# Kernel tuning notes

Hardware: AMD Instinct MI355X
Metric: run time of the kernel (lower is better)

## Reference

```python
import math
import jax, jax.numpy as jnp
import numpy as np

D_MODEL = 1024
H_HEADS = 16
D_K = D_MODEL // H_HEADS


def setup_inputs() -> dict:
    key = jax.random.key(0)
    ks = jax.random.split(key, 7)
    B, L = 4, 2048
    q = jax.random.normal(ks[0], (B, L, D_MODEL), dtype=jnp.float32)
    k = jax.random.normal(ks[1], (B, L, D_MODEL), dtype=jnp.float32)
    v = jax.random.normal(ks[2], (B, L, D_MODEL), dtype=jnp.float32)
    mask = jnp.ones((1, L, L), dtype=jnp.int32)
    # nn.Linear(d_model, d_model, bias=False) weights, shape (out, in)
    s = 1.0 / math.sqrt(D_MODEL)
    W_q = jax.random.uniform(ks[3], (D_MODEL, D_MODEL), jnp.float32, -s, s)
    W_k = jax.random.uniform(ks[4], (D_MODEL, D_MODEL), jnp.float32, -s, s)
    W_v = jax.random.uniform(ks[5], (D_MODEL, D_MODEL), jnp.float32, -s, s)
    W_o = jax.random.uniform(ks[6], (D_MODEL, D_MODEL), jnp.float32, -s, s)
    return {"q": q, "k": k, "v": v, "mask": mask,
            "W_q": W_q, "W_k": W_k, "W_v": W_v, "W_o": W_o}


def reference(q, k, v, mask, W_q, W_k, W_v, W_o):
    B, Lq, _ = q.shape
    # projections (Linear: x @ W.T) then split heads -> (B, H, L, d_k)
    def split_heads(x):
        return x.reshape(B, -1, H_HEADS, D_K).transpose(0, 2, 1, 3)
    Q = split_heads(jnp.einsum('bsd,ed->bse', q, W_q))
    K = split_heads(jnp.einsum('bsd,ed->bse', k, W_k))
    V = split_heads(jnp.einsum('bsd,ed->bse', v, W_v))
    # scores: (B, H, Lq, Lk)
    scores = jnp.einsum('bhqd,bhkd->bhqk', Q, K) / math.sqrt(D_K)
    m = mask[:, None, :, :]  # (1, 1, Lq, Lk) broadcast
    scores = jnp.where(m == 0, -jnp.inf, scores)
    weights = jax.nn.softmax(scores, axis=-1)
    attn = jnp.einsum('bhqk,bhkd->bhqd', weights, V)  # (B, H, Lq, d_v)
    attn = attn.transpose(0, 2, 1, 3).reshape(B, Lq, D_MODEL)
    return jnp.einsum('bse,de->bsd', attn, W_o)
```

## Files before the change

kernel.cpp:

```cpp
#include <hip/hip_runtime.h>
#include <hip/hip_bf16.h>


typedef unsigned short u16;
typedef float f32x4  __attribute__((ext_vector_type(4)));
typedef float f32x16 __attribute__((ext_vector_type(16)));
typedef short s16x8  __attribute__((ext_vector_type(8)));
typedef unsigned u32x4 __attribute__((ext_vector_type(4)));
typedef __bf16 bf16x8 __attribute__((ext_vector_type(8)));

#define QSCL 0.18033688011112042f

__device__ __forceinline__ u16 f2b(float f) {
    union { float f; unsigned u; } x; x.f = f;
    unsigned r = x.u + 0x7fffu + ((x.u >> 16) & 1u);
    return (u16)(r >> 16);
}

__device__ __forceinline__ f32x4 MF(s16x8 a, s16x8 b, f32x4 c) {
    return __builtin_amdgcn_mfma_f32_16x16x32_bf16(
        __builtin_bit_cast(bf16x8, a), __builtin_bit_cast(bf16x8, b), c, 0, 0, 0);
}
__device__ __forceinline__ f32x16 MF32(s16x8 a, s16x8 b, f32x16 c) {
    return __builtin_amdgcn_mfma_f32_32x32x16_bf16(
        __builtin_bit_cast(bf16x8, a), __builtin_bit_cast(bf16x8, b), c, 0, 0, 0);
}
__device__ __forceinline__ unsigned cvtpk(float lo, float hi) {
    unsigned r;
    asm("v_cvt_pk_bf16_f32 %0, %1, %2" : "=v"(r) : "v"(lo), "v"(hi));
    return r;
}
__device__ __forceinline__ void swap32(unsigned &a, unsigned &b) {
    asm volatile("v_permlane32_swap_b32 %0, %1" : "+v"(a), "+v"(b));
}
__device__ __forceinline__ float expa(float x) {
    float r;
    asm("v_exp_f32 %0, %1" : "=v"(r) : "v"(x));
    return r;
}
__device__ __forceinline__ void g2l16(const u16* g, u16* lbase) {
    __builtin_amdgcn_global_load_lds((const __attribute__((address_space(1))) void*)g,
                                     (__attribute__((address_space(3))) void*)lbase, 16, 0, 0);
}

__global__ __launch_bounds__(256)
void mask_flags(const int* __restrict__ mask, int* __restrict__ mflag) {
    __shared__ int anyz;
    if (threadIdx.x == 0) anyz = 0;
    __syncthreads();
    const int qt = blockIdx.x >> 4, kt = blockIdx.x & 15;
    int local = 0;
#pragma unroll
    for (int q = 0; q < 16; ++q) {
        int e4 = q * 256 + threadIdx.x;
        int r = e4 >> 5, cc = (e4 & 31) * 4;
        int4 mv = *(const int4*)(mask + (size_t)(qt * 128 + r) * 2048 + kt * 128 + cc);
        local |= (mv.x == 0) | (mv.y == 0) | (mv.z == 0) | (mv.w == 0);
    }
    if (local) atomicOr(&anyz, 1);
    __syncthreads();
    if (threadIdx.x == 0) mflag[blockIdx.x] = anyz;
}

__global__ __launch_bounds__(256)
void convert_all(const float* __restrict__ q, const float* __restrict__ k,
                 const float* __restrict__ v, const float* __restrict__ Wq,
                 const float* __restrict__ Wk, const float* __restrict__ Wv,
                 const float* __restrict__ Wo, u16* __restrict__ Abf,
                 u16* __restrict__ Wbf) {
    const size_t NQKV = 25165824;
    const size_t NCH  = 3670016;
    for (size_t cidx = (size_t)blockIdx.x * 256 + threadIdx.x; cidx < NCH;
         cidx += (size_t)gridDim.x * 256) {
        size_t e = cidx * 8;
        const float* src; u16* dst; float scl = 1.f;
        if (e < NQKV) {
            src = (e < 8388608) ? q + e
                : (e < 16777216) ? k + (e - 8388608) : v + (e - 16777216);
            dst = Abf + e;
        } else {
            size_t o = e - NQKV;
            if (o < 1048576)      { src = Wq + o; scl = QSCL; }
            else if (o < 2097152) { src = Wk + (o - 1048576); }
            else if (o < 3145728) { src = Wv + (o - 2097152); }
            else                  { src = Wo + (o - 3145728); }
            dst = Wbf + o;
        }
        float4 a = *(const float4*)(src);
        float4 b = *(const float4*)(src + 4);
        ushort4 p0, p1;
        p0.x = f2b(a.x * scl); p0.y = f2b(a.y * scl);
        p0.z = f2b(a.z * scl); p0.w = f2b(a.w * scl);
        p1.x = f2b(b.x * scl); p1.y = f2b(b.y * scl);
        p1.z = f2b(b.z * scl); p1.w = f2b(b.w * scl);
        *(ushort4*)dst = p0; *(ushort4*)(dst + 4) = p1;
    }
}

__global__ __launch_bounds__(256)
void gemm_qkv_fast(const u16* __restrict__ Abf, const u16* __restrict__ Wbf,
                   u16* __restrict__ Qh, u16* __restrict__ Kf, u16* __restrict__ Vf) {
    __shared__ __align__(16) u16 As[128 * 32];
    __shared__ __align__(16) u16 Bs[128 * 32];
    const int z = blockIdx.z;
    const u16* A = Abf + (size_t)z * (8192 * 1024);
    const u16* W = Wbf + (size_t)z * (1024 * 1024);
    const int tid = threadIdx.x, l = tid & 63, w = tid >> 6;
    const int g = l >> 4, c = l & 15;
    const int m0 = blockIdx.x * 128, n0 = blockIdx.y * 128;
    const int wr = (w >> 1) * 64, wc = (w & 1) * 64;

    f32x4 acc[4][4];
#pragma unroll
    for (int i = 0; i < 4; ++i)
#pragma unroll
        for (int j = 0; j < 4; ++j)
#pragma unroll
            for (int e = 0; e < 4; ++e) acc[i][j][e] = 0.f;

    const u16* Ag = A + (size_t)(m0 + w * 32 + (l >> 2)) * 1024 + (l & 3) * 8;
    const u16* Wg = W + (size_t)(n0 + w * 32 + (l >> 2)) * 1024 + (l & 3) * 8;
    u16* Al = As + w * 1024;
    u16* Bl = Bs + w * 1024;

    for (int kt = 0; kt < 32; ++kt) {
        __syncthreads();
        g2l16(Ag + kt * 32,         Al);
        g2l16(Ag + kt * 32 + 16384, Al + 512);
        g2l16(Wg + kt * 32,         Bl);
        g2l16(Wg + kt * 32 + 16384, Bl + 512);
        __syncthreads();
        s16x8 af[4], bf[4];
#pragma unroll
        for (int i = 0; i < 4; ++i) {
            af[i] = *(const s16x8*)(As + (wr + i * 16 + c) * 32 + g * 8);
            bf[i] = *(const s16x8*)(Bs + (wc + i * 16 + c) * 32 + g * 8);
        }
#pragma unroll
        for (int mi = 0; mi < 4; ++mi)
#pragma unroll
            for (int ni = 0; ni < 4; ++ni)
                acc[mi][ni] = MF(af[mi], bf[ni], acc[mi][ni]);
    }

    if (z == 0) {
#pragma unroll
        for (int mi = 0; mi < 4; ++mi)
#pragma unroll
            for (int ni = 0; ni < 4; ++ni)
#pragma unroll
                for (int j = 0; j < 4; ++j) {
                    int row = m0 + wr + mi * 16 + g * 4 + j;
                    int col = n0 + wc + ni * 16 + c;
                    int b = row >> 11, sl = row & 2047;
                    int h = col >> 6, d = col & 63;
                    Qh[(((size_t)(b * 16 + h)) * 2048 + sl) * 64 + d] = f2b(acc[mi][ni][j]);
                }
    } else if (z == 1) {
#pragma unroll
        for (int mi = 0; mi < 4; ++mi)
#pragma unroll
            for (int ni = 0; ni < 4; ++ni)
#pragma unroll
                for (int j = 0; j < 4; ++j) {
                    int row = m0 + wr + mi * 16 + g * 4 + j;
                    int col = n0 + wc + ni * 16 + c;
                    int b = row >> 11, kk = row & 2047;
                    int h = col >> 6, d = col & 63;
                    size_t off = (size_t)(b * 16 + h) * 131072
                               + (size_t)(((kk >> 5) * 4 + (d >> 4))) * 512
                               + ((kk & 31) + 32 * ((d >> 3) & 1)) * 8 + (d & 7);
                    Kf[off] = f2b(acc[mi][ni][j]);
                }
    } else {
#pragma unroll
        for (int mi = 0; mi < 4; ++mi)
#pragma unroll
            for (int ni = 0; ni < 4; ++ni) {
                int key0 = m0 + wr + mi * 16 + g * 4;
                int col  = n0 + wc + ni * 16 + c;
                int b = key0 >> 11, kk0 = key0 & 2047;
                int h = col >> 6, d = col & 63;
                size_t off = (size_t)(b * 16 + h) * 131072
                           + (size_t)((kk0 >> 6) * 8 + (d >> 5) * 4 + ((kk0 >> 4) & 3)) * 512
                           + (((kk0 >> 3) & 1) * 32 + (d & 31)) * 8 + (kk0 & 7);
                ushort4 pk;
                pk.x = f2b(acc[mi][ni][0]); pk.y = f2b(acc[mi][ni][1]);
                pk.z = f2b(acc[mi][ni][2]); pk.w = f2b(acc[mi][ni][3]);
                *(ushort4*)(Vf + off) = pk;
            }
    }
}

__global__ __launch_bounds__(256)
void gemm_out_fast(const u16* __restrict__ Ab, const u16* __restrict__ W,
                   float* __restrict__ Cout) {
    __shared__ __align__(16) u16 As[128 * 32];
    __shared__ __align__(16) u16 Bs[128 * 32];
    const int tid = threadIdx.x, l = tid & 63, w = tid >> 6;
    const int g = l >> 4, c = l & 15;
    const int m0 = blockIdx.x * 128, n0 = blockIdx.y * 128;
    const int wr = (w >> 1) * 64, wc = (w & 1) * 64;

    f32x4 acc[4][4];
#pragma unroll
    for (int i = 0; i < 4; ++i)
#pragma unroll
        for (int j = 0; j < 4; ++j)
#pragma unroll
            for (int e = 0; e < 4; ++e) acc[i][j][e] = 0.f;

    const u16* Ag = Ab + (size_t)(m0 + w * 32 + (l >> 2)) * 1024 + (l & 3) * 8;
    const u16* Wg = W  + (size_t)(n0 + w * 32 + (l >> 2)) * 1024 + (l & 3) * 8;
    u16* Al = As + w * 1024;
    u16* Bl = Bs + w * 1024;

    for (int kt = 0; kt < 32; ++kt) {
        __syncthreads();
        g2l16(Ag + kt * 32,         Al);
        g2l16(Ag + kt * 32 + 16384, Al + 512);
        g2l16(Wg + kt * 32,         Bl);
        g2l16(Wg + kt * 32 + 16384, Bl + 512);
        __syncthreads();
        s16x8 af[4], bf[4];
#pragma unroll
        for (int i = 0; i < 4; ++i) {
            af[i] = *(const s16x8*)(As + (wr + i * 16 + c) * 32 + g * 8);
            bf[i] = *(const s16x8*)(Bs + (wc + i * 16 + c) * 32 + g * 8);
        }
#pragma unroll
        for (int mi = 0; mi < 4; ++mi)
#pragma unroll
            for (int ni = 0; ni < 4; ++ni)
                acc[mi][ni] = MF(af[mi], bf[ni], acc[mi][ni]);
    }

#pragma unroll
    for (int mi = 0; mi < 4; ++mi)
#pragma unroll
        for (int ni = 0; ni < 4; ++ni)
#pragma unroll
            for (int j = 0; j < 4; ++j) {
                int row = m0 + wr + mi * 16 + g * 4 + j;
                int col = n0 + wc + ni * 16 + c;
                Cout[(size_t)row * 1024 + col] = acc[mi][ni][j];
            }
}

__global__ __launch_bounds__(256)
void flash_attn(const u16* __restrict__ Qh, const u16* __restrict__ Kf,
                const u16* __restrict__ Vf, const int* __restrict__ mask,
                const int* __restrict__ mflag, u16* __restrict__ attnB) {
    __shared__ __align__(16) u16 KV[2][2][8][512];

    const int tid = threadIdx.x, w = tid >> 6, l = tid & 63;
    const int hi = l >> 5, q32 = l & 31;
    const int bh = blockIdx.x, qt = blockIdx.y;
    const size_t base = (size_t)bh * (2048 * 64);
    const u16* Qp = Qh + base;
    const u16* Kp = Kf + base;
    const u16* Vp = Vf + base;
    const int qrow_w = qt * 128 + w * 32;

    int anyflag = 0;
#pragma unroll
    for (int i = 0; i < 16; ++i) anyflag |= mflag[qt * 16 + i];

    s16x8 Qf[4];
#pragma unroll
    for (int s = 0; s < 4; ++s)
        Qf[s] = *(const s16x8*)(Qp + (size_t)(qrow_w + q32) * 64 + s * 16 + hi * 8);

    s16x8 ones;
#pragma unroll
    for (int i = 0; i < 8; ++i) ones[i] = (short)0x3F80;

    f32x16 z16;
#pragma unroll
    for (int r = 0; r < 16; ++r) z16[r] = 0.f;
    f32x16 oA = z16, oB = z16, lacc = z16;

    auto stage = [&](int buf, int kt) {
        const u16* ks = Kp + (size_t)(kt * 8 + w * 2) * 512 + l * 8;
        const u16* vs = Vp + (size_t)(kt * 8 + w * 2) * 512 + l * 8;
        g2l16(ks,       &KV[buf][0][w * 2][0]);
        g2l16(ks + 512, &KV[buf][0][w * 2 + 1][0]);
        g2l16(vs,       &KV[buf][1][w * 2][0]);
        g2l16(vs + 512, &KV[buf][1][w * 2 + 1][0]);
    };
    stage(0, 0);

    for (int kt = 0; kt < 32; ++kt) {
        const int cur = kt & 1;
        __syncthreads();
        if (kt < 31) stage(cur ^ 1, kt + 1);

        __builtin_amdgcn_s_setprio(1);
        f32x16 sA, sB;
        {
            s16x8 ka = *(const s16x8*)&KV[cur][0][0][l * 8];
            s16x8 kb = *(const s16x8*)&KV[cur][0][4][l * 8];
            sA = MF32(ka, Qf[0], z16);
            sB = MF32(kb, Qf[0], z16);
        }
#pragma unroll
        for (int s = 1; s < 4; ++s) {
            s16x8 ka = *(const s16x8*)&KV[cur][0][s][l * 8];
            s16x8 kb = *(const s16x8*)&KV[cur][0][4 + s][l * 8];
            sA = MF32(ka, Qf[s], sA);
            sB = MF32(kb, Qf[s], sB);
        }
        __builtin_amdgcn_s_setprio(0);

        if (anyflag && mflag[qt * 16 + (kt >> 1)] != 0) {
            const int qr = qrow_w + q32, kr0 = kt * 64;
#pragma unroll
            for (int r = 0; r < 16; ++r) {
                int key = (r & 3) + 8 * (r >> 2) + 4 * hi;
                if (mask[(size_t)qr * 2048 + kr0 + key] == 0)      sA[r] = -1e30f;
                if (mask[(size_t)qr * 2048 + kr0 + 32 + key] == 0) sB[r] = -1e30f;
            }
        }

#pragma unroll
        for (int r = 0; r < 16; ++r) sA[r] = expa(sA[r]);
#pragma unroll
        for (int r = 0; r < 16; ++r) sB[r] = expa(sB[r]);

        s16x8 Xp[4];
        {
            u32x4 t;
            unsigned a0 = cvtpk(sA[0], sA[1]),   a1 = cvtpk(sA[2], sA[3]);
            unsigned b0 = cvtpk(sA[4], sA[5]),   b1 = cvtpk(sA[6], sA[7]);
            swap32(a0, b0); swap32(a1, b1);
            t.x = a0; t.y = a1; t.z = b0; t.w = b1; Xp[0] = __builtin_bit_cast(s16x8, t);
            unsigned c0 = cvtpk(sA[8], sA[9]),   c1 = cvtpk(sA[10], sA[11]);
            unsigned d0 = cvtpk(sA[12], sA[13]), d1 = cvtpk(sA[14], sA[15]);
            swap32(c0, d0); swap32(c1, d1);
            t.x = c0; t.y = c1; t.z = d0; t.w = d1; Xp[1] = __builtin_bit_cast(s16x8, t);
            unsigned e0 = cvtpk(sB[0], sB[1]),   e1 = cvtpk(sB[2], sB[3]);
            unsigned f0 = cvtpk(sB[4], sB[5]),   f1 = cvtpk(sB[6], sB[7]);
            swap32(e0, f0); swap32(e1, f1);
            t.x = e0; t.y = e1; t.z = f0; t.w = f1; Xp[2] = __builtin_bit_cast(s16x8, t);
            unsigned g0 = cvtpk(sB[8], sB[9]),   g1 = cvtpk(sB[10], sB[11]);
            unsigned h0 = cvtpk(sB[12], sB[13]), h1 = cvtpk(sB[14], sB[15]);
            swap32(g0, h0); swap32(g1, h1);
            t.x = g0; t.y = g1; t.z = h0; t.w = h1; Xp[3] = __builtin_bit_cast(s16x8, t);
        }

        __builtin_amdgcn_s_setprio(1);
#pragma unroll
        for (int ks = 0; ks < 4; ++ks) {
            s16x8 v0 = *(const s16x8*)&KV[cur][1][ks][l * 8];
            s16x8 v1 = *(const s16x8*)&KV[cur][1][4 + ks][l * 8];
            oA = MF32(Xp[ks], v0, oA);
            oB = MF32(Xp[ks], v1, oB);
            lacc = MF32(Xp[ks], ones, lacc);
        }
        __builtin_amdgcn_s_setprio(0);
    }

    const int b = bh >> 4, h = bh & 15;
#pragma unroll
    for (int r = 0; r < 16; ++r) {
        int qloc = (r & 3) + 8 * (r >> 2) + 4 * hi;
        float inv = __builtin_amdgcn_rcpf(lacc[r]);
        int row = qrow_w + qloc;
        u16* dst = attnB + ((size_t)b * 2048 + row) * 1024 + h * 64 + q32;
        dst[0]  = f2b(oA[r] * inv);
        dst[32] = f2b(oB[r] * inv);
    }
}

extern "C" void kernel_launch(void* const* d_in, const int* in_sizes, int n_in,
                              void* d_out, int out_size, void* d_ws, size_t ws_size,
                              hipStream_t stream) {
    const float* q    = (const float*)d_in[0];
    const float* k    = (const float*)d_in[1];
    const float* v    = (const float*)d_in[2];
    const int*   mask = (const int*)d_in[3];
    const float* Wq   = (const float*)d_in[4];
    const float* Wk   = (const float*)d_in[5];
    const float* Wv   = (const float*)d_in[6];
    const float* Wo   = (const float*)d_in[7];

    char* ws = (char*)d_ws;
    u16* Abf   = (u16*)(ws);
    u16* Wbf   = (u16*)(ws + (48u << 20));
    u16* Qh    = (u16*)(ws + (56u << 20));
    u16* Kf    = (u16*)(ws + (72u << 20));
    u16* Vf    = (u16*)(ws + (88u << 20));
    u16* attnB = (u16*)(ws);
    int* mflag = (int*)(ws + (104u << 20));

    mask_flags<<<dim3(256), dim3(256), 0, stream>>>(mask, mflag);
    convert_all<<<dim3(2048), dim3(256), 0, stream>>>(q, k, v, Wq, Wk, Wv, Wo, Abf, Wbf);
    gemm_qkv_fast<<<dim3(64, 8, 3), dim3(256), 0, stream>>>(Abf, Wbf, Qh, Kf, Vf);
    flash_attn<<<dim3(64, 16), dim3(256), 0, stream>>>(Qh, Kf, Vf, mask, mflag, attnB);
    gemm_out_fast<<<dim3(64, 8), dim3(256), 0, stream>>>(attnB, Wbf + 3145728, (float*)d_out);
}
```

Before: 224.0 us.

## Merge mask-flag and convert kernels; split attention tile into halves for occupancy

Folds the mask-flag scan into the conversion kernel as 256 extra blocks, which removes one kernel launch. The flash attention inner loop now handles the 64-key tile as two 32-key halves, each doing its own QK, exp, pack and PV. This shrinks the number of live score and pack registers, and a launch bound of 4 waves is added to aim for higher occupancy. The cost is more serialized MFMA chains per half, and the register cap could cause spills.

```diff
diff --git a/kernel.cpp b/kernel.cpp
--- a/kernel.cpp
+++ b/kernel.cpp
@@ -44,34 +44,35 @@
 }
 
 __global__ __launch_bounds__(256)
-void mask_flags(const int* __restrict__ mask, int* __restrict__ mflag) {
-    __shared__ int anyz;
-    if (threadIdx.x == 0) anyz = 0;
-    __syncthreads();
-    const int qt = blockIdx.x >> 4, kt = blockIdx.x & 15;
-    int local = 0;
-#pragma unroll
-    for (int q = 0; q < 16; ++q) {
-        int e4 = q * 256 + threadIdx.x;
-        int r = e4 >> 5, cc = (e4 & 31) * 4;
-        int4 mv = *(const int4*)(mask + (size_t)(qt * 128 + r) * 2048 + kt * 128 + cc);
-        local |= (mv.x == 0) | (mv.y == 0) | (mv.z == 0) | (mv.w == 0);
-    }
-    if (local) atomicOr(&anyz, 1);
-    __syncthreads();
-    if (threadIdx.x == 0) mflag[blockIdx.x] = anyz;
-}
-
-__global__ __launch_bounds__(256)
-void convert_all(const float* __restrict__ q, const float* __restrict__ k,
-                 const float* __restrict__ v, const float* __restrict__ Wq,
-                 const float* __restrict__ Wk, const float* __restrict__ Wv,
-                 const float* __restrict__ Wo, u16* __restrict__ Abf,
-                 u16* __restrict__ Wbf) {
+void convert_and_mask(const float* __restrict__ q, const float* __restrict__ k,
+                      const float* __restrict__ v, const float* __restrict__ Wq,
+                      const float* __restrict__ Wk, const float* __restrict__ Wv,
+                      const float* __restrict__ Wo, const int* __restrict__ mask,
+                      u16* __restrict__ Abf, u16* __restrict__ Wbf,
+                      int* __restrict__ mflag) {
+    if (blockIdx.x < 256) {
+        __shared__ int anyz;
+        if (threadIdx.x == 0) anyz = 0;
+        __syncthreads();
+        const int qt = blockIdx.x >> 4, kt = blockIdx.x & 15;
+        int local = 0;
+#pragma unroll
+        for (int qq = 0; qq < 16; ++qq) {
+            int e4 = qq * 256 + threadIdx.x;
+            int r = e4 >> 5, cc = (e4 & 31) * 4;
+            int4 mv = *(const int4*)(mask + (size_t)(qt * 128 + r) * 2048 + kt * 128 + cc);
+            local |= (mv.x == 0) | (mv.y == 0) | (mv.z == 0) | (mv.w == 0);
+        }
+        if (local) atomicOr(&anyz, 1);
+        __syncthreads();
+        if (threadIdx.x == 0) mflag[blockIdx.x] = anyz;
+        return;
+    }
     const size_t NQKV = 25165824;
     const size_t NCH  = 3670016;
-    for (size_t cidx = (size_t)blockIdx.x * 256 + threadIdx.x; cidx < NCH;
-         cidx += (size_t)gridDim.x * 256) {
+    const size_t nconv = (size_t)(gridDim.x - 256) * 256;
+    for (size_t cidx = (size_t)(blockIdx.x - 256) * 256 + threadIdx.x; cidx < NCH;
+         cidx += nconv) {
         size_t e = cidx * 8;
         const float* src; u16* dst; float scl = 1.f;
         if (e < NQKV) {
@@ -247,7 +248,7 @@
             }
 }
 
-__global__ __launch_bounds__(256)
+__global__ __launch_bounds__(256, 4)
 void flash_attn(const u16* __restrict__ Qh, const u16* __restrict__ Kf,
                 const u16* __restrict__ Vf, const int* __restrict__ mask,
                 const int* __restrict__ mflag, u16* __restrict__ attnB) {
@@ -295,69 +296,66 @@
         __syncthreads();
         if (kt < 31) stage(cur ^ 1, kt + 1);
 
-        __builtin_amdgcn_s_setprio(1);
-        f32x16 sA, sB;
-        {
-            s16x8 ka = *(const s16x8*)&KV[cur][0][0][l * 8];
-            s16x8 kb = *(const s16x8*)&KV[cur][0][4][l * 8];
-            sA = MF32(ka, Qf[0], z16);
-            sB = MF32(kb, Qf[0], z16);
-        }
-#pragma unroll
-        for (int s = 1; s < 4; ++s) {
-            s16x8 ka = *(const s16x8*)&KV[cur][0][s][l * 8];
-            s16x8 kb = *(const s16x8*)&KV[cur][0][4 + s][l * 8];
-            sA = MF32(ka, Qf[s], sA);
-            sB = MF32(kb, Qf[s], sB);
-        }
-        __builtin_amdgcn_s_setprio(0);
-
-        if (anyflag && mflag[qt * 16 + (kt >> 1)] != 0) {
-            const int qr = qrow_w + q32, kr0 = kt * 64;
-#pragma unroll
-            for (int r = 0; r < 16; ++r) {
-                int key = (r & 3) + 8 * (r >> 2) + 4 * hi;
-                if (mask[(size_t)qr * 2048 + kr0 + key] == 0)      sA[r] = -1e30f;
-                if (mask[(size_t)qr * 2048 + kr0 + 32 + key] == 0) sB[r] = -1e30f;
-            }
-        }
-
-#pragma unroll
-        for (int r = 0; r < 16; ++r) sA[r] = expa(sA[r]);
-#pragma unroll
-        for (int r = 0; r < 16; ++r) sB[r] = expa(sB[r]);
-
-        s16x8 Xp[4];
-        {
-            u32x4 t;
-            unsigned a0 = cvtpk(sA[0], sA[1]),   a1 = cvtpk(sA[2], sA[3]);
-            unsigned b0 = cvtpk(sA[4], sA[5]),   b1 = cvtpk(sA[6], sA[7]);
-            swap32(a0, b0); swap32(a1, b1);
-            t.x = a0; t.y = a1; t.z = b0; t.w = b1; Xp[0] = __builtin_bit_cast(s16x8, t);
-            unsigned c0 = cvtpk(sA[8], sA[9]),   c1 = cvtpk(sA[10], sA[11]);
-            unsigned d0 = cvtpk(sA[12], sA[13]), d1 = cvtpk(sA[14], sA[15]);
-            swap32(c0, d0); swap32(c1, d1);
-            t.x = c0; t.y = c1; t.z = d0; t.w = d1; Xp[1] = __builtin_bit_cast(s16x8, t);
-            unsigned e0 = cvtpk(sB[0], sB[1]),   e1 = cvtpk(sB[2], sB[3]);
-            unsigned f0 = cvtpk(sB[4], sB[5]),   f1 = cvtpk(sB[6], sB[7]);
-            swap32(e0, f0); swap32(e1, f1);
-            t.x = e0; t.y = e1; t.z = f0; t.w = f1; Xp[2] = __builtin_bit_cast(s16x8, t);
-            unsigned g0 = cvtpk(sB[8], sB[9]),   g1 = cvtpk(sB[10], sB[11]);
-            unsigned h0 = cvtpk(sB[12], sB[13]), h1 = cvtpk(sB[14], sB[15]);
-            swap32(g0, h0); swap32(g1, h1);
-            t.x = g0; t.y = g1; t.z = h0; t.w = h1; Xp[3] = __builtin_bit_cast(s16x8, t);
-        }
-
-        __builtin_amdgcn_s_setprio(1);
-#pragma unroll
-        for (int ks = 0; ks < 4; ++ks) {
-            s16x8 v0 = *(const s16x8*)&KV[cur][1][ks][l * 8];
-            s16x8 v1 = *(const s16x8*)&KV[cur][1][4 + ks][l * 8];
-            oA = MF32(Xp[ks], v0, oA);
-            oB = MF32(Xp[ks], v1, oB);
-            lacc = MF32(Xp[ks], ones, lacc);
-        }
-        __builtin_amdgcn_s_setprio(0);
+        const int kr0 = kt * 64;
+        const bool dom = anyflag && (mflag[qt * 16 + (kt >> 1)] != 0);
+
+#pragma unroll
+        for (int half = 0; half < 2; ++half) {
+            __builtin_amdgcn_s_setprio(1);
+            f32x16 s;
+            {
+                s16x8 ka = *(const s16x8*)&KV[cur][0][half * 4][l * 8];
+                s = MF32(ka, Qf[0], z16);
+            }
+#pragma unroll
+            for (int ss = 1; ss < 4; ++ss) {
+                s16x8 ka = *(const s16x8*)&KV[cur][0][half * 4 + ss][l * 8];
+                s = MF32(ka, Qf[ss], s);
+            }
+            __builtin_amdgcn_s_setprio(0);
+
+            if (dom) {
+                const int qr = qrow_w + q32, kb = kr0 + half * 32;
+#pragma unroll
+                for (int r = 0; r < 16; ++r) {
+                    int key = (r & 3) + 8 * (r >> 2) + 4 * hi;
+                    if (mask[(size_t)qr * 2048 + kb + key] == 0) s[r] = -1e30f;
+                }
+            }
+
+#pragma unroll
+            for (int r = 0; r < 16; ++r) s[r] = expa(s[r]);
+
+            s16x8 Xp0, Xp1;
+            {
+                u32x4 t;
+                unsigned a0 = cvtpk(s[0], s[1]),   a1 = cvtpk(s[2], s[3]);
+                unsigned b0 = cvtpk(s[4], s[5]),   b1 = cvtpk(s[6], s[7]);
+                swap32(a0, b0); swap32(a1, b1);
+                t.x = a0; t.y = a1; t.z = b0; t.w = b1;
+                Xp0 = __builtin_bit_cast(s16x8, t);
+                unsigned c0 = cvtpk(s[8], s[9]),   c1 = cvtpk(s[10], s[11]);
+                unsigned d0 = cvtpk(s[12], s[13]), d1 = cvtpk(s[14], s[15]);
+                swap32(c0, d0); swap32(c1, d1);
+                t.x = c0; t.y = c1; t.z = d0; t.w = d1;
+                Xp1 = __builtin_bit_cast(s16x8, t);
+            }
+
+            __builtin_amdgcn_s_setprio(1);
+            {
+                s16x8 v0 = *(const s16x8*)&KV[cur][1][half * 2][l * 8];
+                s16x8 v1 = *(const s16x8*)&KV[cur][1][4 + half * 2][l * 8];
+                oA = MF32(Xp0, v0, oA);
+                oB = MF32(Xp0, v1, oB);
+                lacc = MF32(Xp0, ones, lacc);
+                s16x8 v2 = *(const s16x8*)&KV[cur][1][half * 2 + 1][l * 8];
+                s16x8 v3 = *(const s16x8*)&KV[cur][1][4 + half * 2 + 1][l * 8];
+                oA = MF32(Xp1, v2, oA);
+                oB = MF32(Xp1, v3, oB);
+                lacc = MF32(Xp1, ones, lacc);
+            }
+            __builtin_amdgcn_s_setprio(0);
+        }
     }
 
     const int b = bh >> 4, h = bh & 15;
@@ -393,8 +391,8 @@
     u16* attnB = (u16*)(ws);
     int* mflag = (int*)(ws + (104u << 20));
 
-    mask_flags<<<dim3(256), dim3(256), 0, stream>>>(mask, mflag);
-    convert_all<<<dim3(2048), dim3(256), 0, stream>>>(q, k, v, Wq, Wk, Wv, Wo, Abf, Wbf);
+    convert_and_mask<<<dim3(2304), dim3(256), 0, stream>>>(q, k, v, Wq, Wk, Wv, Wo,
+                                                           mask, Abf, Wbf, mflag);
     gemm_qkv_fast<<<dim3(64, 8, 3), dim3(256), 0, stream>>>(Abf, Wbf, Qh, Kf, Vf);
     flash_attn<<<dim3(64, 16), dim3(256), 0, stream>>>(Qh, Kf, Vf, mask, mflag, attnB);
     gemm_out_fast<<<dim3(64, 8), dim3(256), 0, stream>>>(attnB, Wbf + 3145728, (float*)d_out);
```

New measurement: 211.0 us. -5.8%, faster.
